# Kernel tuning notes

Measured on AMD Instinct MI355X. Metric: run time of the kernel, lower is better.

## Reference

```python
import jax, jax.numpy as jnp
import numpy as np

MIDC = 256
HEADS = 16
HEADC = MIDC // HEADS
EPS = 1e-5


def _layernorm(x, w, b):
    # Faithful to the custom torch LayerNorm: unbiased std (ddof=1) and
    # division by (std + eps), NOT sqrt(var + eps).
    mean = jnp.mean(x, axis=-1, keepdims=True)
    std = jnp.std(x, axis=-1, keepdims=True, ddof=1)
    return w * (x - mean) / (std + EPS) + b


def setup_inputs() -> dict:
    key = jax.random.key(0)
    ks = jax.random.split(key, 3)
    B, HW = 8, 16384
    x = jax.random.normal(ks[0], (B, HW, MIDC), dtype=jnp.float32)
    W_qkv = jax.random.normal(ks[1], (3 * MIDC, MIDC), dtype=jnp.float32) * 0.02
    b_qkv = jnp.zeros((3 * MIDC,), dtype=jnp.float32)
    kln_w = jnp.ones((HEADS, 1, HEADC), dtype=jnp.float32)
    kln_b = jnp.zeros((HEADS, 1, HEADC), dtype=jnp.float32)
    vln_w = jnp.ones((HEADS, 1, HEADC), dtype=jnp.float32)
    vln_b = jnp.zeros((HEADS, 1, HEADC), dtype=jnp.float32)
    W_proj = jax.random.normal(ks[2], (MIDC, MIDC), dtype=jnp.float32) * 0.02
    b_proj = jnp.zeros((MIDC,), dtype=jnp.float32)
    return {"x": x, "W_qkv": W_qkv, "b_qkv": b_qkv,
            "kln_w": kln_w, "kln_b": kln_b, "vln_w": vln_w, "vln_b": vln_b,
            "W_proj": W_proj, "b_proj": b_proj}


def reference(x, W_qkv, b_qkv, kln_w, kln_b, vln_w, vln_b, W_proj, b_proj):
    B, HW, C = x.shape
    bias = x
    # QKV projection -> [B, heads, HW, 3*headc]
    qkv = (jnp.einsum('bnc,oc->bno', x, W_qkv) + b_qkv)
    qkv = qkv.reshape(B, HW, HEADS, 3 * HEADC).transpose(0, 2, 1, 3)
    q, k, v = jnp.split(qkv, 3, axis=-1)  # each [B, heads, HW, headc]
    k = _layernorm(k, kln_w, kln_b)
    v = _layernorm(v, vln_w, vln_b)
    # linear attention: kv = k^T v / HW, then q @ kv
    kv = jnp.einsum('bhnd,bhne->bhde', k, v) / HW  # [B, heads, headc, headc]
    out = jnp.einsum('bhnd,bhde->bhne', q, kv)     # [B, heads, HW, headc]
    out = out.transpose(0, 2, 1, 3).reshape(B, HW, C)
    ret = out + bias
    proj = jnp.einsum('bnc,oc->bno', ret, W_proj) + b_proj
    return jax.nn.gelu(proj, approximate=False) + bias
```

## Files before the change

### kernel.cpp

```cpp
#include <hip/hip_runtime.h>
#include <hip/hip_bf16.h>
#include <math.h>


#define EPSF 1e-5f

typedef __bf16 bf16x8 __attribute__((ext_vector_type(8)));
typedef __bf16 bf16x4 __attribute__((ext_vector_type(4)));
typedef float  f32x4  __attribute__((ext_vector_type(4)));

__global__ void k0_prep(const float* __restrict__ Wqkv, const float* __restrict__ Wproj,
                        __bf16* __restrict__ Wkv, __bf16* __restrict__ Wp,
                        float* __restrict__ kv) {
  int idx = blockIdx.x * 256 + threadIdx.x;
  if (idx < 32768) kv[idx] = 0.f;
  {
    int r = idx >> 8, c = idx & 255;
    int half = r >> 8;
    int rr = r & 255;
    int h = rr >> 4, d = rr & 15;
    Wkv[idx] = (__bf16)Wqkv[(h*48 + 16 + half*16 + d)*256 + c];
  }
  if (idx < 65536) Wp[idx] = (__bf16)Wproj[idx];
}

__launch_bounds__(512, 4)
__global__ void k1a(const float* __restrict__ x, const __bf16* __restrict__ Wkv,
                    const float* __restrict__ bqkv,
                    const float* __restrict__ klnw, const float* __restrict__ klnb,
                    const float* __restrict__ vlnw, const float* __restrict__ vlnb,
                    float* __restrict__ kvout) {
  __shared__ __align__(16) char smem[70656];
  __bf16 (*xs)[264] = reinterpret_cast<__bf16(*)[264]>(smem);
  const int tid = threadIdx.x;
  const int w = tid >> 6, l = tid & 63, lr = l & 15, g = l >> 4;
  __bf16 (*tTk)[72] = reinterpret_cast<__bf16(*)[72]>(smem + 33792 + w*4608);
  __bf16 (*tTv)[64] = reinterpret_cast<__bf16(*)[64]>(smem + w*4096);

  const long row0 = (long)blockIdx.x * 64;
  const int b = (int)(row0 >> 14);

  #pragma unroll
  for (int i = 0; i < 8; ++i) {
    int idx = tid + i*512;
    int r = idx >> 6, c4 = (idx & 63) << 2;
    f32x4 v = *reinterpret_cast<const f32x4*>(x + (row0 + r)*256 + c4);
    bf16x4 pk; pk[0]=(__bf16)v[0]; pk[1]=(__bf16)v[1]; pk[2]=(__bf16)v[2]; pk[3]=(__bf16)v[3];
    *reinterpret_cast<bf16x4*>(&xs[r][c4]) = pk;
  }

  bf16x8 wk[2][8];
  #pragma unroll
  for (int cb=0;cb<2;cb++) {
    const __bf16* wp = Wkv + (size_t)(w*32 + cb*16 + lr)*256 + g*8;
    #pragma unroll
    for (int kc=0;kc<8;kc++) wk[cb][kc] = *reinterpret_cast<const bf16x8*>(wp + kc*32);
  }
  __syncthreads();

  f32x4 acc[2][4];
  for (int cb=0;cb<2;cb++) for (int rb=0;rb<4;rb++)
    for (int j=0;j<4;j++) acc[cb][rb][j]=0.f;
  #pragma unroll
  for (int kc = 0; kc < 8; ++kc) {
    const int kb = kc*32 + g*8;
    bf16x8 bf_[4];
    #pragma unroll
    for (int rb=0;rb<4;rb++)
      bf_[rb] = *reinterpret_cast<const bf16x8*>(&xs[rb*16+lr][kb]);
    #pragma unroll
    for (int cb=0;cb<2;cb++)
      #pragma unroll
      for (int rb=0;rb<4;rb++)
        acc[cb][rb] = __builtin_amdgcn_mfma_f32_16x16x32_bf16(wk[cb][kc], bf_[rb], acc[cb][rb], 0,0,0);
  }

  bf16x8 wv[2][8];
  #pragma unroll
  for (int cb=0;cb<2;cb++) {
    const __bf16* wp = Wkv + (size_t)(256 + w*32 + cb*16 + lr)*256 + g*8;
    #pragma unroll
    for (int kc=0;kc<8;kc++) wv[cb][kc] = *reinterpret_cast<const bf16x8*>(wp + kc*32);
  }

  #pragma unroll
  for (int cb=0;cb<2;cb++) {
    const int h = 2*w + cb;
    const f32x4 bb  = *reinterpret_cast<const f32x4*>(bqkv + h*48 + 16 + 4*g);
    const f32x4 lwv = *reinterpret_cast<const f32x4*>(klnw + h*16 + 4*g);
    const f32x4 lbv = *reinterpret_cast<const f32x4*>(klnb + h*16 + 4*g);
    #pragma unroll
    for (int rb=0;rb<4;rb++) {
      float v0 = acc[cb][rb][0] + bb[0];
      float v1 = acc[cb][rb][1] + bb[1];
      float v2 = acc[cb][rb][2] + bb[2];
      float v3 = acc[cb][rb][3] + bb[3];
      float sum = v0+v1+v2+v3;
      sum += __shfl_xor(sum, 16); sum += __shfl_xor(sum, 32);
      const float mu = sum * 0.0625f;
      const float d0=v0-mu, d1=v1-mu, d2=v2-mu, d3=v3-mu;
      float q = d0*d0 + d1*d1 + d2*d2 + d3*d3;
      q += __shfl_xor(q, 16); q += __shfl_xor(q, 32);
      const float sc = __frsqrt_rn(q * (1.f/15.f));
      const int rr = rb*16 + lr;
      tTk[cb*16 + 4*g+0][rr] = (__bf16)(lwv[0]*d0*sc + lbv[0]);
      tTk[cb*16 + 4*g+1][rr] = (__bf16)(lwv[1]*d1*sc + lbv[1]);
      tTk[cb*16 + 4*g+2][rr] = (__bf16)(lwv[2]*d2*sc + lbv[2]);
      tTk[cb*16 + 4*g+3][rr] = (__bf16)(lwv[3]*d3*sc + lbv[3]);
    }
  }

  for (int cb=0;cb<2;cb++) for (int rb=0;rb<4;rb++)
    for (int j=0;j<4;j++) acc[cb][rb][j]=0.f;
  #pragma unroll
  for (int kc = 0; kc < 8; ++kc) {
    const int kb = kc*32 + g*8;
    bf16x8 bf_[4];
    #pragma unroll
    for (int rb=0;rb<4;rb++)
      bf_[rb] = *reinterpret_cast<const bf16x8*>(&xs[rb*16+lr][kb]);
    #pragma unroll
    for (int cb=0;cb<2;cb++)
      #pragma unroll
      for (int rb=0;rb<4;rb++)
        acc[cb][rb] = __builtin_amdgcn_mfma_f32_16x16x32_bf16(wv[cb][kc], bf_[rb], acc[cb][rb], 0,0,0);
  }
  __syncthreads();

  #pragma unroll
  for (int cb=0;cb<2;cb++) {
    const int h = 2*w + cb;
    const f32x4 bb  = *reinterpret_cast<const f32x4*>(bqkv + h*48 + 32 + 4*g);
    const f32x4 lwv = *reinterpret_cast<const f32x4*>(vlnw + h*16 + 4*g);
    const f32x4 lbv = *reinterpret_cast<const f32x4*>(vlnb + h*16 + 4*g);
    #pragma unroll
    for (int rb=0;rb<4;rb++) {
      float v0 = acc[cb][rb][0] + bb[0];
      float v1 = acc[cb][rb][1] + bb[1];
      float v2 = acc[cb][rb][2] + bb[2];
      float v3 = acc[cb][rb][3] + bb[3];
      float sum = v0+v1+v2+v3;
      sum += __shfl_xor(sum, 16); sum += __shfl_xor(sum, 32);
      const float mu = sum * 0.0625f;
      const float d0=v0-mu, d1=v1-mu, d2=v2-mu, d3=v3-mu;
      float q = d0*d0 + d1*d1 + d2*d2 + d3*d3;
      q += __shfl_xor(q, 16); q += __shfl_xor(q, 32);
      const float sc = __frsqrt_rn(q * (1.f/15.f));
      const int rr = rb*16 + lr;
      tTv[cb*16 + 4*g+0][rr ^ (((4*g+0)&7)<<3)] = (__bf16)(lwv[0]*d0*sc + lbv[0]);
      tTv[cb*16 + 4*g+1][rr ^ (((4*g+1)&7)<<3)] = (__bf16)(lwv[1]*d1*sc + lbv[1]);
      tTv[cb*16 + 4*g+2][rr ^ (((4*g+2)&7)<<3)] = (__bf16)(lwv[2]*d2*sc + lbv[2]);
      tTv[cb*16 + 4*g+3][rr ^ (((4*g+3)&7)<<3)] = (__bf16)(lwv[3]*d3*sc + lbv[3]);
    }
  }

  #pragma unroll
  for (int hh=0; hh<2; ++hh) {
    f32x4 c; c[0]=0.f; c[1]=0.f; c[2]=0.f; c[3]=0.f;
    #pragma unroll
    for (int ch=0; ch<2; ++ch) {
      const int s = ch*32 + g*8;
      bf16x8 a  = *reinterpret_cast<const bf16x8*>(&tTk[hh*16 + lr][s]);
      bf16x8 bv = *reinterpret_cast<const bf16x8*>(&tTv[hh*16 + lr][s ^ ((lr&7)<<3)]);
      c = __builtin_amdgcn_mfma_f32_16x16x32_bf16(a, bv, c, 0,0,0);
    }
    float* dst = kvout + ((size_t)(b*16 + 2*w + hh) << 8);
    #pragma unroll
    for (int j=0;j<4;j++)
      atomicAdd(dst + (4*g+j)*16 + lr, c[j]);
  }
}

__global__ void k2_weff(const float* __restrict__ Wqkv, const float* __restrict__ bqkv,
                        const float* __restrict__ kvin,
                        __bf16* __restrict__ Wqe, float* __restrict__ beff) {
  const int b = blockIdx.x >> 4, h = blockIdx.x & 15;
  const int c = threadIdx.x;
  __shared__ float kvs[16][16];
  kvs[c >> 4][c & 15] = kvin[(b*16 + h)*256 + c] * (1.f/16384.f);
  __syncthreads();
  #pragma unroll 4
  for (int e=0;e<16;e++) {
    float acc = 0.f;
    #pragma unroll
    for (int d=0; d<16; d++)
      acc += kvs[d][e] * Wqkv[(h*48 + d)*256 + c];
    Wqe[((size_t)b*256 + h*16 + e)*256 + c] = (__bf16)acc;
  }
  if (c < 16) {
    float acc = 0.f;
    #pragma unroll
    for (int d=0; d<16; d++) acc += kvs[d][c] * bqkv[h*48 + d];
    beff[b*256 + h*16 + c] = acc;
  }
}

__launch_bounds__(512, 4)
__global__ void k3_fused(const float* __restrict__ x, const __bf16* __restrict__ Wqe,
                         const float* __restrict__ beff, const __bf16* __restrict__ Wp,
                         const float* __restrict__ bproj, float* __restrict__ out) {
  __shared__ __align__(16) __bf16 xs[64][264];
  __shared__ __align__(16) char rsraw[33792];
  __bf16 (*rs)[264] = reinterpret_cast<__bf16(*)[264]>(rsraw);
  float  (*fst)[260] = reinterpret_cast<float(*)[260]>(rsraw);
  const int tid = threadIdx.x;
  const long browg = (long)blockIdx.x * 64;
  const int b = (int)(browg >> 14);
  const int w = tid>>6, l = tid&63, lr = l&15, g = l>>4;

  #pragma unroll
  for (int i = 0; i < 8; ++i) {
    int idx = tid + i*512;
    int r = idx >> 6, c4 = (idx & 63) << 2;
    f32x4 v = *reinterpret_cast<const f32x4*>(x + (browg + r)*256 + c4);
    bf16x4 pk; pk[0]=(__bf16)v[0]; pk[1]=(__bf16)v[1]; pk[2]=(__bf16)v[2]; pk[3]=(__bf16)v[3];
    *reinterpret_cast<bf16x4*>(&xs[r][c4]) = pk;
  }

  const __bf16* Bq = Wqe + (size_t)b*65536;
  bf16x8 wq[2][8];
  #pragma unroll
  for (int cb=0;cb<2;cb++) {
    const __bf16* wp = Bq + (size_t)(w*32 + cb*16 + lr)*256 + g*8;
    #pragma unroll
    for (int kc=0;kc<8;kc++) wq[cb][kc] = *reinterpret_cast<const bf16x8*>(wp + kc*32);
  }
  __syncthreads();

  f32x4 acc[2][4];
  for (int cb=0;cb<2;cb++) for (int rb=0;rb<4;rb++)
    for (int j=0;j<4;j++) acc[cb][rb][j]=0.f;
  #pragma unroll
  for (int kc=0;kc<8;kc++) {
    const int kb = kc*32 + g*8;
    bf16x8 bf_[4];
    #pragma unroll
    for (int rb=0;rb<4;rb++)
      bf_[rb] = *reinterpret_cast<const bf16x8*>(&xs[rb*16+lr][kb]);
    #pragma unroll
    for (int cb=0;cb<2;cb++)
      #pragma unroll
      for (int rb=0;rb<4;rb++)
        acc[cb][rb] = __builtin_amdgcn_mfma_f32_16x16x32_bf16(wq[cb][kc], bf_[rb], acc[cb][rb], 0,0,0);
  }

  bf16x8 wpj[2][8];
  #pragma unroll
  for (int cb=0;cb<2;cb++) {
    const __bf16* wp = Wp + (size_t)(w*32 + cb*16 + lr)*256 + g*8;
    #pragma unroll
    for (int kc=0;kc<8;kc++) wpj[cb][kc] = *reinterpret_cast<const bf16x8*>(wp + kc*32);
  }

  #pragma unroll
  for (int cb=0;cb<2;cb++) {
    const int c0 = w*32 + cb*16 + 4*g;
    const f32x4 be = *reinterpret_cast<const f32x4*>(beff + b*256 + c0);
    #pragma unroll
    for (int rb=0;rb<4;rb++) {
      const int r = rb*16 + lr;
      bf16x4 xv = *reinterpret_cast<const bf16x4*>(&xs[r][c0]);
      bf16x4 pk;
      #pragma unroll
      for (int j=0;j<4;j++)
        pk[j] = (__bf16)(acc[cb][rb][j] + be[j] + (float)xv[j]);
      *reinterpret_cast<bf16x4*>(&rs[r][c0]) = pk;
    }
  }
  __syncthreads();

  f32x4 acc2[2][4];
  for (int cb=0;cb<2;cb++) for (int rb=0;rb<4;rb++)
    for (int j=0;j<4;j++) acc2[cb][rb][j]=0.f;
  #pragma unroll
  for (int kc=0;kc<8;kc++) {
    const int kb = kc*32 + g*8;
    bf16x8 bf_[4];
    #pragma unroll
    for (int rb=0;rb<4;rb++)
      bf_[rb] = *reinterpret_cast<const bf16x8*>(&rs[rb*16+lr][kb]);
    #pragma unroll
    for (int cb=0;cb<2;cb++)
      #pragma unroll
      for (int rb=0;rb<4;rb++)
        acc2[cb][rb] = __builtin_amdgcn_mfma_f32_16x16x32_bf16(wpj[cb][kc], bf_[rb], acc2[cb][rb], 0,0,0);
  }
  __syncthreads();

  #pragma unroll
  for (int half=0; half<2; ++half) {
    #pragma unroll
    for (int cb=0;cb<2;cb++) {
      const int c0 = w*32 + cb*16 + 4*g;
      const f32x4 bp4 = *reinterpret_cast<const f32x4*>(bproj + c0);
      #pragma unroll
      for (int rbh=0;rbh<2;rbh++) {
        const int rb = half*2 + rbh;
        const int r = rb*16 + lr;
        bf16x4 xv = *reinterpret_cast<const bf16x4*>(&xs[r][c0]);
        f32x4 o;
        #pragma unroll
        for (int j=0;j<4;j++) {
          float z = acc2[cb][rb][j] + bp4[j];
          o[j] = 0.5f*z*(1.f + erff(z*0.70710678118f)) + (float)xv[j];
        }
        *reinterpret_cast<f32x4*>(&fst[r - half*32][c0]) = o;
      }
    }
    __syncthreads();
    #pragma unroll
    for (int i=0;i<4;i++) {
      int idx = tid + i*512;
      int r32 = idx >> 6, c4 = (idx & 63) << 2;
      f32x4 v = *reinterpret_cast<const f32x4*>(&fst[r32][c4]);
      *reinterpret_cast<f32x4*>(out + (browg + half*32 + r32)*256 + c4) = v;
    }
    if (half == 0) __syncthreads();
  }
}

extern "C" void kernel_launch(void* const* d_in, const int* in_sizes, int n_in,
                              void* d_out, int out_size, void* d_ws, size_t ws_size,
                              hipStream_t stream) {
  const float* x    = (const float*)d_in[0];
  const float* Wqkv = (const float*)d_in[1];
  const float* bqkv = (const float*)d_in[2];
  const float* klnw = (const float*)d_in[3];
  const float* klnb = (const float*)d_in[4];
  const float* vlnw = (const float*)d_in[5];
  const float* vlnb = (const float*)d_in[6];
  const float* Wproj= (const float*)d_in[7];
  const float* bproj= (const float*)d_in[8];
  float* out = (float*)d_out;

  char* ws = (char*)d_ws;
  __bf16* Wkv = (__bf16*)(ws);
  __bf16* Wp  = (__bf16*)(ws + 262144);
  float*  kv  = (float*) (ws + 393216);
  __bf16* Wqe = (__bf16*)(ws + 524288);
  float*  beff= (float*) (ws + 1572864);

  k0_prep <<<512, 256, 0, stream>>>(Wqkv, Wproj, Wkv, Wp, kv);
  k1a     <<<2048, 512, 0, stream>>>(x, Wkv, bqkv, klnw, klnb, vlnw, vlnb, kv);
  k2_weff <<<128, 256, 0, stream>>>(Wqkv, bqkv, kv, Wqe, beff);
  k3_fused<<<2048, 512, 0, stream>>>(x, Wqe, beff, Wp, bproj, out);
}
```

Baseline: 193.2 us.

## Spread kv atomics across eight slices and merge K/V projection loops

Result: no change. 193.4 us (+0.1%).

```diff
diff --git a/kernel.cpp b/kernel.cpp
--- a/kernel.cpp
+++ b/kernel.cpp
@@ -11,10 +11,10 @@
 
 __global__ void k0_prep(const float* __restrict__ Wqkv, const float* __restrict__ Wproj,
                         __bf16* __restrict__ Wkv, __bf16* __restrict__ Wp,
-                        float* __restrict__ kv) {
+                        float* __restrict__ kv8) {
   int idx = blockIdx.x * 256 + threadIdx.x;
-  if (idx < 32768) kv[idx] = 0.f;
-  {
+  kv8[idx] = 0.f;
+  if (idx < 131072) {
     int r = idx >> 8, c = idx & 255;
     int half = r >> 8;
     int rr = r & 255;
@@ -29,7 +29,7 @@
                     const float* __restrict__ bqkv,
                     const float* __restrict__ klnw, const float* __restrict__ klnb,
                     const float* __restrict__ vlnw, const float* __restrict__ vlnb,
-                    float* __restrict__ kvout) {
+                    float* __restrict__ kv8) {
   __shared__ __align__(16) char smem[70656];
   __bf16 (*xs)[264] = reinterpret_cast<__bf16(*)[264]>(smem);
   const int tid = threadIdx.x;
@@ -48,53 +48,42 @@
     bf16x4 pk; pk[0]=(__bf16)v[0]; pk[1]=(__bf16)v[1]; pk[2]=(__bf16)v[2]; pk[3]=(__bf16)v[3];
     *reinterpret_cast<bf16x4*>(&xs[r][c4]) = pk;
   }
-
-  bf16x8 wk[2][8];
-  #pragma unroll
-  for (int cb=0;cb<2;cb++) {
-    const __bf16* wp = Wkv + (size_t)(w*32 + cb*16 + lr)*256 + g*8;
-    #pragma unroll
-    for (int kc=0;kc<8;kc++) wk[cb][kc] = *reinterpret_cast<const bf16x8*>(wp + kc*32);
-  }
-  __syncthreads();
-
-  f32x4 acc[2][4];
-  for (int cb=0;cb<2;cb++) for (int rb=0;rb<4;rb++)
-    for (int j=0;j<4;j++) acc[cb][rb][j]=0.f;
+  __syncthreads();
+
+  f32x4 acc[4][4];
+  for (int s=0;s<4;s++) for (int rb=0;rb<4;rb++)
+    for (int j=0;j<4;j++) acc[s][rb][j]=0.f;
   #pragma unroll
   for (int kc = 0; kc < 8; ++kc) {
     const int kb = kc*32 + g*8;
-    bf16x8 bf_[4];
+    bf16x8 wfr[4], bf_[4];
+    #pragma unroll
+    for (int s=0;s<4;s++) {
+      const int wrow = ((s>>1)<<8) + w*32 + ((s&1)<<4) + lr;
+      wfr[s] = *reinterpret_cast<const bf16x8*>(Wkv + (size_t)wrow*256 + kb);
+    }
     #pragma unroll
     for (int rb=0;rb<4;rb++)
       bf_[rb] = *reinterpret_cast<const bf16x8*>(&xs[rb*16+lr][kb]);
     #pragma unroll
-    for (int cb=0;cb<2;cb++)
+    for (int s=0;s<4;s++)
       #pragma unroll
       for (int rb=0;rb<4;rb++)
-        acc[cb][rb] = __builtin_amdgcn_mfma_f32_16x16x32_bf16(wk[cb][kc], bf_[rb], acc[cb][rb], 0,0,0);
-  }
-
-  bf16x8 wv[2][8];
-  #pragma unroll
-  for (int cb=0;cb<2;cb++) {
-    const __bf16* wp = Wkv + (size_t)(256 + w*32 + cb*16 + lr)*256 + g*8;
-    #pragma unroll
-    for (int kc=0;kc<8;kc++) wv[cb][kc] = *reinterpret_cast<const bf16x8*>(wp + kc*32);
-  }
-
-  #pragma unroll
-  for (int cb=0;cb<2;cb++) {
-    const int h = 2*w + cb;
+        acc[s][rb] = __builtin_amdgcn_mfma_f32_16x16x32_bf16(wfr[s], bf_[rb], acc[s][rb], 0,0,0);
+  }
+
+  #pragma unroll
+  for (int s=0;s<2;s++) {
+    const int h = 2*w + s;
     const f32x4 bb  = *reinterpret_cast<const f32x4*>(bqkv + h*48 + 16 + 4*g);
     const f32x4 lwv = *reinterpret_cast<const f32x4*>(klnw + h*16 + 4*g);
     const f32x4 lbv = *reinterpret_cast<const f32x4*>(klnb + h*16 + 4*g);
     #pragma unroll
     for (int rb=0;rb<4;rb++) {
-      float v0 = acc[cb][rb][0] + bb[0];
-      float v1 = acc[cb][rb][1] + bb[1];
-      float v2 = acc[cb][rb][2] + bb[2];
-      float v3 = acc[cb][rb][3] + bb[3];
+      float v0 = acc[s][rb][0] + bb[0];
+      float v1 = acc[s][rb][1] + bb[1];
+      float v2 = acc[s][rb][2] + bb[2];
+      float v3 = acc[s][rb][3] + bb[3];
       float sum = v0+v1+v2+v3;
       sum += __shfl_xor(sum, 16); sum += __shfl_xor(sum, 32);
       const float mu = sum * 0.0625f;
@@ -103,42 +92,27 @@
       q += __shfl_xor(q, 16); q += __shfl_xor(q, 32);
       const float sc = __frsqrt_rn(q * (1.f/15.f));
       const int rr = rb*16 + lr;
-      tTk[cb*16 + 4*g+0][rr] = (__bf16)(lwv[0]*d0*sc + lbv[0]);
-      tTk[cb*16 + 4*g+1][rr] = (__bf16)(lwv[1]*d1*sc + lbv[1]);
-      tTk[cb*16 + 4*g+2][rr] = (__bf16)(lwv[2]*d2*sc + lbv[2]);
-      tTk[cb*16 + 4*g+3][rr] = (__bf16)(lwv[3]*d3*sc + lbv[3]);
-    }
-  }
-
-  for (int cb=0;cb<2;cb++) for (int rb=0;rb<4;rb++)
-    for (int j=0;j<4;j++) acc[cb][rb][j]=0.f;
-  #pragma unroll
-  for (int kc = 0; kc < 8; ++kc) {
-    const int kb = kc*32 + g*8;
-    bf16x8 bf_[4];
-    #pragma unroll
-    for (int rb=0;rb<4;rb++)
-      bf_[rb] = *reinterpret_cast<const bf16x8*>(&xs[rb*16+lr][kb]);
-    #pragma unroll
-    for (int cb=0;cb<2;cb++)
-      #pragma unroll
-      for (int rb=0;rb<4;rb++)
-        acc[cb][rb] = __builtin_amdgcn_mfma_f32_16x16x32_bf16(wv[cb][kc], bf_[rb], acc[cb][rb], 0,0,0);
-  }
-  __syncthreads();
-
-  #pragma unroll
-  for (int cb=0;cb<2;cb++) {
-    const int h = 2*w + cb;
+      tTk[s*16 + 4*g+0][rr] = (__bf16)(lwv[0]*d0*sc + lbv[0]);
+      tTk[s*16 + 4*g+1][rr] = (__bf16)(lwv[1]*d1*sc + lbv[1]);
+      tTk[s*16 + 4*g+2][rr] = (__bf16)(lwv[2]*d2*sc + lbv[2]);
+      tTk[s*16 + 4*g+3][rr] = (__bf16)(lwv[3]*d3*sc + lbv[3]);
+    }
+  }
+  __syncthreads();
+
+  #pragma unroll
+  for (int s=2;s<4;s++) {
+    const int cbl = s - 2;
+    const int h = 2*w + cbl;
     const f32x4 bb  = *reinterpret_cast<const f32x4*>(bqkv + h*48 + 32 + 4*g);
     const f32x4 lwv = *reinterpret_cast<const f32x4*>(vlnw + h*16 + 4*g);
     const f32x4 lbv = *reinterpret_cast<const f32x4*>(vlnb + h*16 + 4*g);
     #pragma unroll
     for (int rb=0;rb<4;rb++) {
-      float v0 = acc[cb][rb][0] + bb[0];
-      float v1 = acc[cb][rb][1] + bb[1];
-      float v2 = acc[cb][rb][2] + bb[2];
-      float v3 = acc[cb][rb][3] + bb[3];
+      float v0 = acc[s][rb][0] + bb[0];
+      float v1 = acc[s][rb][1] + bb[1];
+      float v2 = acc[s][rb][2] + bb[2];
+      float v3 = acc[s][rb][3] + bb[3];
       float sum = v0+v1+v2+v3;
       sum += __shfl_xor(sum, 16); sum += __shfl_xor(sum, 32);
       const float mu = sum * 0.0625f;
@@ -147,13 +121,14 @@
       q += __shfl_xor(q, 16); q += __shfl_xor(q, 32);
       const float sc = __frsqrt_rn(q * (1.f/15.f));
       const int rr = rb*16 + lr;
-      tTv[cb*16 + 4*g+0][rr ^ (((4*g+0)&7)<<3)] = (__bf16)(lwv[0]*d0*sc + lbv[0]);
-      tTv[cb*16 + 4*g+1][rr ^ (((4*g+1)&7)<<3)] = (__bf16)(lwv[1]*d1*sc + lbv[1]);
-      tTv[cb*16 + 4*g+2][rr ^ (((4*g+2)&7)<<3)] = (__bf16)(lwv[2]*d2*sc + lbv[2]);
-      tTv[cb*16 + 4*g+3][rr ^ (((4*g+3)&7)<<3)] = (__bf16)(lwv[3]*d3*sc + lbv[3]);
-    }
-  }
-
+      tTv[cbl*16 + 4*g+0][rr ^ (((4*g+0)&7)<<3)] = (__bf16)(lwv[0]*d0*sc + lbv[0]);
+      tTv[cbl*16 + 4*g+1][rr ^ (((4*g+1)&7)<<3)] = (__bf16)(lwv[1]*d1*sc + lbv[1]);
+      tTv[cbl*16 + 4*g+2][rr ^ (((4*g+2)&7)<<3)] = (__bf16)(lwv[2]*d2*sc + lbv[2]);
+      tTv[cbl*16 + 4*g+3][rr ^ (((4*g+3)&7)<<3)] = (__bf16)(lwv[3]*d3*sc + lbv[3]);
+    }
+  }
+
+  float* slice = kv8 + (size_t)(blockIdx.x & 7) * 32768;
   #pragma unroll
   for (int hh=0; hh<2; ++hh) {
     f32x4 c; c[0]=0.f; c[1]=0.f; c[2]=0.f; c[3]=0.f;
@@ -164,7 +139,7 @@
       bf16x8 bv = *reinterpret_cast<const bf16x8*>(&tTv[hh*16 + lr][s ^ ((lr&7)<<3)]);
       c = __builtin_amdgcn_mfma_f32_16x16x32_bf16(a, bv, c, 0,0,0);
     }
-    float* dst = kvout + ((size_t)(b*16 + 2*w + hh) << 8);
+    float* dst = slice + ((size_t)(b*16 + 2*w + hh) << 8);
     #pragma unroll
     for (int j=0;j<4;j++)
       atomicAdd(dst + (4*g+j)*16 + lr, c[j]);
@@ -172,12 +147,15 @@
 }
 
 __global__ void k2_weff(const float* __restrict__ Wqkv, const float* __restrict__ bqkv,
-                        const float* __restrict__ kvin,
+                        const float* __restrict__ kv8,
                         __bf16* __restrict__ Wqe, float* __restrict__ beff) {
   const int b = blockIdx.x >> 4, h = blockIdx.x & 15;
   const int c = threadIdx.x;
   __shared__ float kvs[16][16];
-  kvs[c >> 4][c & 15] = kvin[(b*16 + h)*256 + c] * (1.f/16384.f);
+  float acc0 = 0.f;
+  #pragma unroll
+  for (int s=0;s<8;s++) acc0 += kv8[(size_t)s*32768 + (b*16 + h)*256 + c];
+  kvs[c >> 4][c & 15] = acc0 * (1.f/16384.f);
   __syncthreads();
   #pragma unroll 4
   for (int e=0;e<16;e++) {
@@ -336,12 +314,13 @@
   char* ws = (char*)d_ws;
   __bf16* Wkv = (__bf16*)(ws);
   __bf16* Wp  = (__bf16*)(ws + 262144);
-  float*  kv  = (float*) (ws + 393216);
-  __bf16* Wqe = (__bf16*)(ws + 524288);
-  float*  beff= (float*) (ws + 1572864);
-
-  k0_prep <<<512, 256, 0, stream>>>(Wqkv, Wproj, Wkv, Wp, kv);
-  k1a     <<<2048, 512, 0, stream>>>(x, Wkv, bqkv, klnw, klnb, vlnw, vlnb, kv);
-  k2_weff <<<128, 256, 0, stream>>>(Wqkv, bqkv, kv, Wqe, beff);
+  __bf16* Wqe = (__bf16*)(ws + 393216);
+  float*  beff= (float*) (ws + 1441792);
+
+  float* kv8 = (float*)d_out;
+
+  k0_prep <<<1024, 256, 0, stream>>>(Wqkv, Wproj, Wkv, Wp, kv8);
+  k1a     <<<2048, 512, 0, stream>>>(x, Wkv, bqkv, klnw, klnb, vlnw, vlnb, kv8);
+  k2_weff <<<128, 256, 0, stream>>>(Wqkv, bqkv, kv8, Wqe, beff);
   k3_fused<<<2048, 512, 0, stream>>>(x, Wqe, beff, Wp, bproj, out);
 }
```

## Loop k1a over four row tiles with prefetch and deterministic partial kv sums

Applied to the files above, without the earlier changes.

After: 322.7 us. +67.0%, slower.

```diff
diff --git a/kernel.cpp b/kernel.cpp
--- a/kernel.cpp
+++ b/kernel.cpp
@@ -10,10 +10,8 @@
 typedef float  f32x4  __attribute__((ext_vector_type(4)));
 
 __global__ void k0_prep(const float* __restrict__ Wqkv, const float* __restrict__ Wproj,
-                        __bf16* __restrict__ Wkv, __bf16* __restrict__ Wp,
-                        float* __restrict__ kv) {
+                        __bf16* __restrict__ Wkv, __bf16* __restrict__ Wp) {
   int idx = blockIdx.x * 256 + threadIdx.x;
-  if (idx < 32768) kv[idx] = 0.f;
   {
     int r = idx >> 8, c = idx & 255;
     int half = r >> 8;
@@ -29,155 +27,205 @@
                     const float* __restrict__ bqkv,
                     const float* __restrict__ klnw, const float* __restrict__ klnb,
                     const float* __restrict__ vlnw, const float* __restrict__ vlnb,
-                    float* __restrict__ kvout) {
-  __shared__ __align__(16) char smem[70656];
+                    float* __restrict__ part) {
+  __shared__ __align__(16) char smem[66560];
   __bf16 (*xs)[264] = reinterpret_cast<__bf16(*)[264]>(smem);
   const int tid = threadIdx.x;
   const int w = tid >> 6, l = tid & 63, lr = l & 15, g = l >> 4;
-  __bf16 (*tTk)[72] = reinterpret_cast<__bf16(*)[72]>(smem + 33792 + w*4608);
-  __bf16 (*tTv)[64] = reinterpret_cast<__bf16(*)[64]>(smem + w*4096);
-
-  const long row0 = (long)blockIdx.x * 64;
-  const int b = (int)(row0 >> 14);
+  char* pw = smem + 33792 + w*4096;
+
+  const int b  = blockIdx.x >> 6;
+  const long tbase = (long)b*16384 + (long)(blockIdx.x & 63)*256;
 
   #pragma unroll
   for (int i = 0; i < 8; ++i) {
     int idx = tid + i*512;
     int r = idx >> 6, c4 = (idx & 63) << 2;
-    f32x4 v = *reinterpret_cast<const f32x4*>(x + (row0 + r)*256 + c4);
+    f32x4 v = *reinterpret_cast<const f32x4*>(x + (tbase + r)*256 + c4);
     bf16x4 pk; pk[0]=(__bf16)v[0]; pk[1]=(__bf16)v[1]; pk[2]=(__bf16)v[2]; pk[3]=(__bf16)v[3];
     *reinterpret_cast<bf16x4*>(&xs[r][c4]) = pk;
   }
 
-  bf16x8 wk[2][8];
-  #pragma unroll
-  for (int cb=0;cb<2;cb++) {
-    const __bf16* wp = Wkv + (size_t)(w*32 + cb*16 + lr)*256 + g*8;
-    #pragma unroll
-    for (int kc=0;kc<8;kc++) wk[cb][kc] = *reinterpret_cast<const bf16x8*>(wp + kc*32);
-  }
-  __syncthreads();
-
-  f32x4 acc[2][4];
-  for (int cb=0;cb<2;cb++) for (int rb=0;rb<4;rb++)
-    for (int j=0;j<4;j++) acc[cb][rb][j]=0.f;
-  #pragma unroll
-  for (int kc = 0; kc < 8; ++kc) {
-    const int kb = kc*32 + g*8;
-    bf16x8 bf_[4];
-    #pragma unroll
-    for (int rb=0;rb<4;rb++)
-      bf_[rb] = *reinterpret_cast<const bf16x8*>(&xs[rb*16+lr][kb]);
-    #pragma unroll
-    for (int cb=0;cb<2;cb++)
+  f32x4 kvacc[2];
+  for (int j=0;j<4;j++) { kvacc[0][j]=0.f; kvacc[1][j]=0.f; }
+
+  const int h0 = 2*w;
+  const int prr = tid >> 6, prc = (tid & 63) << 2;
+
+  for (int t = 0; t < 4; ++t) {
+    __syncthreads();
+
+    f32x4 pref[6];
+    if (t < 3) {
+      const long rown = tbase + (t+1)*64;
+      #pragma unroll
+      for (int i=0;i<6;i++)
+        pref[i] = *reinterpret_cast<const f32x4*>(x + (rown + prr + i*8)*256 + prc);
+    }
+
+    f32x4 acc[2][4];
+    for (int cb=0;cb<2;cb++) for (int rb=0;rb<4;rb++)
+      for (int j=0;j<4;j++) acc[cb][rb][j]=0.f;
+    #pragma unroll
+    for (int kc = 0; kc < 8; ++kc) {
+      const int kb = kc*32 + g*8;
+      bf16x8 wfr[2], bf_[4];
+      #pragma unroll
+      for (int cb=0;cb<2;cb++)
+        wfr[cb] = *reinterpret_cast<const bf16x8*>(Wkv + (size_t)(w*32 + cb*16 + lr)*256 + kb);
       #pragma unroll
       for (int rb=0;rb<4;rb++)
-        acc[cb][rb] = __builtin_amdgcn_mfma_f32_16x16x32_bf16(wk[cb][kc], bf_[rb], acc[cb][rb], 0,0,0);
-  }
-
-  bf16x8 wv[2][8];
-  #pragma unroll
-  for (int cb=0;cb<2;cb++) {
-    const __bf16* wp = Wkv + (size_t)(256 + w*32 + cb*16 + lr)*256 + g*8;
-    #pragma unroll
-    for (int kc=0;kc<8;kc++) wv[cb][kc] = *reinterpret_cast<const bf16x8*>(wp + kc*32);
-  }
-
-  #pragma unroll
-  for (int cb=0;cb<2;cb++) {
-    const int h = 2*w + cb;
-    const f32x4 bb  = *reinterpret_cast<const f32x4*>(bqkv + h*48 + 16 + 4*g);
-    const f32x4 lwv = *reinterpret_cast<const f32x4*>(klnw + h*16 + 4*g);
-    const f32x4 lbv = *reinterpret_cast<const f32x4*>(klnb + h*16 + 4*g);
-    #pragma unroll
-    for (int rb=0;rb<4;rb++) {
-      float v0 = acc[cb][rb][0] + bb[0];
-      float v1 = acc[cb][rb][1] + bb[1];
-      float v2 = acc[cb][rb][2] + bb[2];
-      float v3 = acc[cb][rb][3] + bb[3];
-      float sum = v0+v1+v2+v3;
-      sum += __shfl_xor(sum, 16); sum += __shfl_xor(sum, 32);
-      const float mu = sum * 0.0625f;
-      const float d0=v0-mu, d1=v1-mu, d2=v2-mu, d3=v3-mu;
-      float q = d0*d0 + d1*d1 + d2*d2 + d3*d3;
-      q += __shfl_xor(q, 16); q += __shfl_xor(q, 32);
-      const float sc = __frsqrt_rn(q * (1.f/15.f));
-      const int rr = rb*16 + lr;
-      tTk[cb*16 + 4*g+0][rr] = (__bf16)(lwv[0]*d0*sc + lbv[0]);
-      tTk[cb*16 + 4*g+1][rr] = (__bf16)(lwv[1]*d1*sc + lbv[1]);
-      tTk[cb*16 + 4*g+2][rr] = (__bf16)(lwv[2]*d2*sc + lbv[2]);
-      tTk[cb*16 + 4*g+3][rr] = (__bf16)(lwv[3]*d3*sc + lbv[3]);
-    }
-  }
-
-  for (int cb=0;cb<2;cb++) for (int rb=0;rb<4;rb++)
-    for (int j=0;j<4;j++) acc[cb][rb][j]=0.f;
-  #pragma unroll
-  for (int kc = 0; kc < 8; ++kc) {
-    const int kb = kc*32 + g*8;
-    bf16x8 bf_[4];
-    #pragma unroll
-    for (int rb=0;rb<4;rb++)
-      bf_[rb] = *reinterpret_cast<const bf16x8*>(&xs[rb*16+lr][kb]);
-    #pragma unroll
-    for (int cb=0;cb<2;cb++)
+        bf_[rb] = *reinterpret_cast<const bf16x8*>(&xs[rb*16+lr][kb]);
+      #pragma unroll
+      for (int cb=0;cb<2;cb++)
+        #pragma unroll
+        for (int rb=0;rb<4;rb++)
+          acc[cb][rb] = __builtin_amdgcn_mfma_f32_16x16x32_bf16(wfr[cb], bf_[rb], acc[cb][rb], 0,0,0);
+    }
+
+    bf16x4 khold[4];
+    #pragma unroll
+    for (int cb=0;cb<2;cb++) {
+      const int h = h0 + cb;
+      const f32x4 bb  = *reinterpret_cast<const f32x4*>(bqkv + h*48 + 16 + 4*g);
+      const f32x4 lwv = *reinterpret_cast<const f32x4*>(klnw + h*16 + 4*g);
+      const f32x4 lbv = *reinterpret_cast<const f32x4*>(klnb + h*16 + 4*g);
+      #pragma unroll
+      for (int rb=0;rb<4;rb++) {
+        float v0 = acc[cb][rb][0] + bb[0];
+        float v1 = acc[cb][rb][1] + bb[1];
+        float v2 = acc[cb][rb][2] + bb[2];
+        float v3 = acc[cb][rb][3] + bb[3];
+        float sum = v0+v1+v2+v3;
+        sum += __shfl_xor(sum, 16); sum += __shfl_xor(sum, 32);
+        const float mu = sum * 0.0625f;
+        const float d0=v0-mu, d1=v1-mu, d2=v2-mu, d3=v3-mu;
+        float q = d0*d0 + d1*d1 + d2*d2 + d3*d3;
+        q += __shfl_xor(q, 16); q += __shfl_xor(q, 32);
+        const float sc = __frsqrt_rn(q * (1.f/15.f));
+        bf16x4 pk;
+        pk[0]=(__bf16)(lwv[0]*d0*sc + lbv[0]); pk[1]=(__bf16)(lwv[1]*d1*sc + lbv[1]);
+        pk[2]=(__bf16)(lwv[2]*d2*sc + lbv[2]); pk[3]=(__bf16)(lwv[3]*d3*sc + lbv[3]);
+        if (cb == 0) {
+          const int cbyte = (2*rb + (lr>>3))*256 + ((lr&7)<<1);
+          *reinterpret_cast<__bf16*>(pw + cbyte + (4*g+0)*16) = pk[0];
+          *reinterpret_cast<__bf16*>(pw + cbyte + (4*g+1)*16) = pk[1];
+          *reinterpret_cast<__bf16*>(pw + cbyte + (4*g+2)*16) = pk[2];
+          *reinterpret_cast<__bf16*>(pw + cbyte + (4*g+3)*16) = pk[3];
+        } else {
+          khold[rb] = pk;
+        }
+      }
+    }
+
+    for (int cb=0;cb<2;cb++) for (int rb=0;rb<4;rb++)
+      for (int j=0;j<4;j++) acc[cb][rb][j]=0.f;
+    #pragma unroll
+    for (int kc = 0; kc < 8; ++kc) {
+      const int kb = kc*32 + g*8;
+      bf16x8 wfr[2], bf_[4];
+      #pragma unroll
+      for (int cb=0;cb<2;cb++)
+        wfr[cb] = *reinterpret_cast<const bf16x8*>(Wkv + (size_t)(256 + w*32 + cb*16 + lr)*256 + kb);
       #pragma unroll
       for (int rb=0;rb<4;rb++)
-        acc[cb][rb] = __builtin_amdgcn_mfma_f32_16x16x32_bf16(wv[cb][kc], bf_[rb], acc[cb][rb], 0,0,0);
-  }
-  __syncthreads();
-
-  #pragma unroll
-  for (int cb=0;cb<2;cb++) {
-    const int h = 2*w + cb;
-    const f32x4 bb  = *reinterpret_cast<const f32x4*>(bqkv + h*48 + 32 + 4*g);
-    const f32x4 lwv = *reinterpret_cast<const f32x4*>(vlnw + h*16 + 4*g);
-    const f32x4 lbv = *reinterpret_cast<const f32x4*>(vlnb + h*16 + 4*g);
-    #pragma unroll
-    for (int rb=0;rb<4;rb++) {
-      float v0 = acc[cb][rb][0] + bb[0];
-      float v1 = acc[cb][rb][1] + bb[1];
-      float v2 = acc[cb][rb][2] + bb[2];
-      float v3 = acc[cb][rb][3] + bb[3];
-      float sum = v0+v1+v2+v3;
-      sum += __shfl_xor(sum, 16); sum += __shfl_xor(sum, 32);
-      const float mu = sum * 0.0625f;
-      const float d0=v0-mu, d1=v1-mu, d2=v2-mu, d3=v3-mu;
-      float q = d0*d0 + d1*d1 + d2*d2 + d3*d3;
-      q += __shfl_xor(q, 16); q += __shfl_xor(q, 32);
-      const float sc = __frsqrt_rn(q * (1.f/15.f));
-      const int rr = rb*16 + lr;
-      tTv[cb*16 + 4*g+0][rr ^ (((4*g+0)&7)<<3)] = (__bf16)(lwv[0]*d0*sc + lbv[0]);
-      tTv[cb*16 + 4*g+1][rr ^ (((4*g+1)&7)<<3)] = (__bf16)(lwv[1]*d1*sc + lbv[1]);
-      tTv[cb*16 + 4*g+2][rr ^ (((4*g+2)&7)<<3)] = (__bf16)(lwv[2]*d2*sc + lbv[2]);
-      tTv[cb*16 + 4*g+3][rr ^ (((4*g+3)&7)<<3)] = (__bf16)(lwv[3]*d3*sc + lbv[3]);
+        bf_[rb] = *reinterpret_cast<const bf16x8*>(&xs[rb*16+lr][kb]);
+      #pragma unroll
+      for (int cb=0;cb<2;cb++)
+        #pragma unroll
+        for (int rb=0;rb<4;rb++)
+          acc[cb][rb] = __builtin_amdgcn_mfma_f32_16x16x32_bf16(wfr[cb], bf_[rb], acc[cb][rb], 0,0,0);
+    }
+
+    #pragma unroll
+    for (int hh=0; hh<2; ++hh) {
+      const int h = h0 + hh;
+      if (hh == 1) {
+        #pragma unroll
+        for (int rb=0;rb<4;rb++) {
+          const int cbyte = (2*rb + (lr>>3))*256 + ((lr&7)<<1);
+          *reinterpret_cast<__bf16*>(pw + cbyte + (4*g+0)*16) = khold[rb][0];
+          *reinterpret_cast<__bf16*>(pw + cbyte + (4*g+1)*16) = khold[rb][1];
+          *reinterpret_cast<__bf16*>(pw + cbyte + (4*g+2)*16) = khold[rb][2];
+          *reinterpret_cast<__bf16*>(pw + cbyte + (4*g+3)*16) = khold[rb][3];
+        }
+      }
+      {
+        const f32x4 bb  = *reinterpret_cast<const f32x4*>(bqkv + h*48 + 32 + 4*g);
+        const f32x4 lwv = *reinterpret_cast<const f32x4*>(vlnw + h*16 + 4*g);
+        const f32x4 lbv = *reinterpret_cast<const f32x4*>(vlnb + h*16 + 4*g);
+        #pragma unroll
+        for (int rb=0;rb<4;rb++) {
+          float v0 = acc[hh][rb][0] + bb[0];
+          float v1 = acc[hh][rb][1] + bb[1];
+          float v2 = acc[hh][rb][2] + bb[2];
+          float v3 = acc[hh][rb][3] + bb[3];
+          float sum = v0+v1+v2+v3;
+          sum += __shfl_xor(sum, 16); sum += __shfl_xor(sum, 32);
+          const float mu = sum * 0.0625f;
+          const float d0=v0-mu, d1=v1-mu, d2=v2-mu, d3=v3-mu;
+          float q = d0*d0 + d1*d1 + d2*d2 + d3*d3;
+          q += __shfl_xor(q, 16); q += __shfl_xor(q, 32);
+          const float sc = __frsqrt_rn(q * (1.f/15.f));
+          const int cbyte = (2*rb + (lr>>3))*256 + ((lr&7)<<1);
+          *reinterpret_cast<__bf16*>(pw + 2048 + cbyte + (4*g+0)*16) = (__bf16)(lwv[0]*d0*sc + lbv[0]);
+          *reinterpret_cast<__bf16*>(pw + 2048 + cbyte + (4*g+1)*16) = (__bf16)(lwv[1]*d1*sc + lbv[1]);
+          *reinterpret_cast<__bf16*>(pw + 2048 + cbyte + (4*g+2)*16) = (__bf16)(lwv[2]*d2*sc + lbv[2]);
+          *reinterpret_cast<__bf16*>(pw + 2048 + cbyte + (4*g+3)*16) = (__bf16)(lwv[3]*d3*sc + lbv[3]);
+        }
+      }
+      #pragma unroll
+      for (int ch=0; ch<2; ++ch) {
+        bf16x8 a  = *reinterpret_cast<const bf16x8*>(pw +        (ch*4+g)*256 + lr*16);
+        bf16x8 bv = *reinterpret_cast<const bf16x8*>(pw + 2048 + (ch*4+g)*256 + lr*16);
+        kvacc[hh] = __builtin_amdgcn_mfma_f32_16x16x32_bf16(a, bv, kvacc[hh], 0,0,0);
+      }
+    }
+
+    __syncthreads();
+
+    if (t < 3) {
+      #pragma unroll
+      for (int i=0;i<6;i++) {
+        bf16x4 pk; pk[0]=(__bf16)pref[i][0]; pk[1]=(__bf16)pref[i][1];
+                   pk[2]=(__bf16)pref[i][2]; pk[3]=(__bf16)pref[i][3];
+        *reinterpret_cast<bf16x4*>(&xs[prr + i*8][prc]) = pk;
+      }
+      const long rown = tbase + (t+1)*64;
+      #pragma unroll
+      for (int i=6;i<8;i++) {
+        f32x4 v = *reinterpret_cast<const f32x4*>(x + (rown + prr + i*8)*256 + prc);
+        bf16x4 pk; pk[0]=(__bf16)v[0]; pk[1]=(__bf16)v[1]; pk[2]=(__bf16)v[2]; pk[3]=(__bf16)v[3];
+        *reinterpret_cast<bf16x4*>(&xs[prr + i*8][prc]) = pk;
+      }
     }
   }
 
   #pragma unroll
   for (int hh=0; hh<2; ++hh) {
-    f32x4 c; c[0]=0.f; c[1]=0.f; c[2]=0.f; c[3]=0.f;
-    #pragma unroll
-    for (int ch=0; ch<2; ++ch) {
-      const int s = ch*32 + g*8;
-      bf16x8 a  = *reinterpret_cast<const bf16x8*>(&tTk[hh*16 + lr][s]);
-      bf16x8 bv = *reinterpret_cast<const bf16x8*>(&tTv[hh*16 + lr][s ^ ((lr&7)<<3)]);
-      c = __builtin_amdgcn_mfma_f32_16x16x32_bf16(a, bv, c, 0,0,0);
-    }
-    float* dst = kvout + ((size_t)(b*16 + 2*w + hh) << 8);
+    float* dst = part + ((size_t)blockIdx.x*16 + h0 + hh)*256;
     #pragma unroll
     for (int j=0;j<4;j++)
-      atomicAdd(dst + (4*g+j)*16 + lr, c[j]);
+      dst[(4*g+j)*16 + lr] = kvacc[hh][j];
   }
 }
 
 __global__ void k2_weff(const float* __restrict__ Wqkv, const float* __restrict__ bqkv,
-                        const float* __restrict__ kvin,
+                        const float* __restrict__ part,
                         __bf16* __restrict__ Wqe, float* __restrict__ beff) {
   const int b = blockIdx.x >> 4, h = blockIdx.x & 15;
   const int c = threadIdx.x;
   __shared__ float kvs[16][16];
-  kvs[c >> 4][c & 15] = kvin[(b*16 + h)*256 + c] * (1.f/16384.f);
+  const float* base = part + ((size_t)(b*64)*16 + h)*256 + c;
+  float a0=0.f, a1=0.f, a2=0.f, a3=0.f;
+  #pragma unroll 4
+  for (int i=0;i<64;i+=4) {
+    a0 += base[(size_t)(i+0)*4096];
+    a1 += base[(size_t)(i+1)*4096];
+    a2 += base[(size_t)(i+2)*4096];
+    a3 += base[(size_t)(i+3)*4096];
+  }
+  kvs[c >> 4][c & 15] = ((a0+a1)+(a2+a3)) * (1.f/16384.f);
   __syncthreads();
   #pragma unroll 4
   for (int e=0;e<16;e++) {
@@ -336,12 +384,13 @@
   char* ws = (char*)d_ws;
   __bf16* Wkv = (__bf16*)(ws);
   __bf16* Wp  = (__bf16*)(ws + 262144);
-  float*  kv  = (float*) (ws + 393216);
-  __bf16* Wqe = (__bf16*)(ws + 524288);
-  float*  beff= (float*) (ws + 1572864);
-
-  k0_prep <<<512, 256, 0, stream>>>(Wqkv, Wproj, Wkv, Wp, kv);
-  k1a     <<<2048, 512, 0, stream>>>(x, Wkv, bqkv, klnw, klnb, vlnw, vlnb, kv);
-  k2_weff <<<128, 256, 0, stream>>>(Wqkv, bqkv, kv, Wqe, beff);
+  __bf16* Wqe = (__bf16*)(ws + 393216);
+  float*  beff= (float*) (ws + 1441792);
+
+  float* part = (float*)d_out;
+
+  k0_prep <<<512, 256, 0, stream>>>(Wqkv, Wproj, Wkv, Wp);
+  k1a     <<<512, 512, 0, stream>>>(x, Wkv, bqkv, klnw, klnb, vlnw, vlnb, part);
+  k2_weff <<<128, 256, 0, stream>>>(Wqkv, bqkv, part, Wqe, beff);
   k3_fused<<<2048, 512, 0, stream>>>(x, Wqe, beff, Wp, bproj, out);
 }
```
